# Optimization experiments

Hardware: AMD Instinct MI355X
Metric: run time of the kernel (lower is better)

## Reference

```python
import jax, jax.numpy as jnp
import numpy as np

TEMP = 0.2
NUM_PATCH, BATCH, DIM = 16, 512, 2048


def _l2_normalize(x, axis=-1, eps=1e-12):
    # matches torch F.normalize: x / max(||x||, eps)
    norm = jnp.linalg.norm(x, axis=axis, keepdims=True)
    return x / jnp.maximum(norm, eps)


def setup_inputs() -> dict:
    key = jax.random.key(0)
    features = jax.random.normal(key, (NUM_PATCH, BATCH, DIM), dtype=jnp.float32)
    return {"features": features}


def reference(features) -> jnp.ndarray:
    P, B, D = features.shape
    # z_avg: mean over the num_patch crops -> [B, D]
    z_avg = _l2_normalize(features.mean(axis=0), axis=1)
    # concat crops along batch -> [P*B, D], then L2 normalize rows
    f = _l2_normalize(features.reshape(P * B, D), axis=1)
    # similarity matrix [P*B, B]
    sim = f @ z_avg.T
    # labels = identity(B) tiled P times along rows => positive of row i is column i % B.
    # CE with target 0 after concat([pos, negs]) == -pos/T + logsumexp(all/T)
    rows = jnp.arange(P * B)
    pos = sim[rows, rows % B]
    logits = sim / TEMP
    loss = jnp.mean(jax.nn.logsumexp(logits, axis=1) - pos / TEMP)
    return loss
```

## Files before the change

kernel.cpp:

```cpp
#include <hip/hip_runtime.h>
#include <hip/hip_bf16.h>
#include <math.h>

#define NP 16
#define NB 512
#define ND 2048
#define NM (NP*NB)
#define BM 64
#define BN 128
#define BK 64
#define NS (ND/BK)
#define NCB (NB/BN)

typedef __attribute__((ext_vector_type(4))) float f32x4;
typedef unsigned int u32;

__device__ inline float dot4(float4 v) {
    return v.x * v.x + v.y * v.y + v.z * v.z + v.w * v.w;
}

#if __has_builtin(__builtin_amdgcn_cvt_pk_fp8_f32)
__device__ inline u32 pack4_fp8(float a, float b, float c, float d) {
    int w = 0;
    w = __builtin_amdgcn_cvt_pk_fp8_f32(a, b, w, false);
    w = __builtin_amdgcn_cvt_pk_fp8_f32(c, d, w, true);
    return (u32)w;
}
#else
#include <hip/hip_fp8.h>
__device__ inline u32 pack4_fp8(float a, float b, float c, float d) {
    u32 w  = (u32)__hip_cvt_float_to_fp8(a, __HIP_SATFINITE, __HIP_E4M3);
    w |= (u32)__hip_cvt_float_to_fp8(b, __HIP_SATFINITE, __HIP_E4M3) << 8;
    w |= (u32)__hip_cvt_float_to_fp8(c, __HIP_SATFINITE, __HIP_E4M3) << 16;
    w |= (u32)__hip_cvt_float_to_fp8(d, __HIP_SATFINITE, __HIP_E4M3) << 24;
    return w;
}
#endif

__global__ __launch_bounds__(512) void prep_kernel(
        const float* __restrict__ feat,
        unsigned char* __restrict__ an,
        unsigned char* __restrict__ zn) {
    const int b = blockIdx.x, tid = threadIdx.x;
    const int lane = tid & 63, wv = tid >> 6;
    const float4* feat4 = (const float4*)feat;

    float4 zp[8];
#pragma unroll
    for (int it = 0; it < 8; ++it) zp[it] = make_float4(0.f, 0.f, 0.f, 0.f);

#pragma unroll
    for (int j = 0; j < 2; ++j) {
        const int p = wv * 2 + j;
        const size_t row = (size_t)p * NB + b;
        const float4* rp = feat4 + row * (ND / 4);
        float4 rv[8];
        float ss = 0.f;
#pragma unroll
        for (int it = 0; it < 8; ++it) {
            rv[it] = rp[it * 64 + lane];
            ss += dot4(rv[it]);
            zp[it].x += rv[it].x; zp[it].y += rv[it].y;
            zp[it].z += rv[it].z; zp[it].w += rv[it].w;
        }
#pragma unroll
        for (int off = 32; off > 0; off >>= 1) ss += __shfl_xor(ss, off);
        const float inv = 1.f / fmaxf(sqrtf(ss), 1e-12f);
        u32* wp = (u32*)(an + row * ND);
#pragma unroll
        for (int it = 0; it < 8; ++it)
            wp[it * 64 + lane] = pack4_fp8(rv[it].x * inv, rv[it].y * inv,
                                           rv[it].z * inv, rv[it].w * inv);
    }

    __shared__ float4 zl[8][512];
#pragma unroll
    for (int it = 0; it < 8; ++it) zl[wv][it * 64 + lane] = zp[it];
    __syncthreads();

    float4 z = zl[0][tid];
#pragma unroll
    for (int v = 1; v < 8; ++v) {
        float4 t = zl[v][tid];
        z.x += t.x; z.y += t.y; z.z += t.z; z.w += t.w;
    }
    float ss = dot4(z);
#pragma unroll
    for (int off = 32; off > 0; off >>= 1) ss += __shfl_xor(ss, off);
    __shared__ float wpart[8];
    __shared__ float invz_s;
    if (lane == 0) wpart[wv] = ss;
    __syncthreads();
    if (tid == 0) {
        float t = 0.f;
#pragma unroll
        for (int v = 0; v < 8; ++v) t += wpart[v];
        invz_s = 1.f / fmaxf(sqrtf(t), 1e-12f);
    }
    __syncthreads();
    const float iz = invz_s;
    ((u32*)(zn + (size_t)b * ND))[tid] =
        pack4_fp8(z.x * iz, z.y * iz, z.z * iz, z.w * iz);
}

__global__ __launch_bounds__(256, 2) void gemm_loss_kernel(
        const unsigned char* __restrict__ an,
        const unsigned char* __restrict__ zn,
        float* __restrict__ pmax_g,
        float* __restrict__ psum_g,
        float* __restrict__ ppos_g) {
    __shared__ __align__(16) unsigned char abuf[3 * BM * BK];
    __shared__ __align__(16) unsigned char bbuf[3 * BN * BK];
    __shared__ float sm_max[BM][2];
    __shared__ float sm_sum[BM][2];
    __shared__ float sm_pos[BM];

    const int tid  = threadIdx.x;
    const int lane = tid & 63;
    const int w    = tid >> 6;
    const int wr   = w >> 1;
    const int wc   = w & 1;
    const int l15  = lane & 15;
    const int l4   = lane >> 4;
    const int cb   = blockIdx.x & (NCB - 1);
    const int brow = (blockIdx.x >> 2) * BM;
    const int bcol = cb * BN;

    f32x4 acc[2][4] = {};

    const int sra = tid >> 2;
    const int sca = (tid & 3) ^ ((sra >> 2) & 3);
    const unsigned char* asrc = an + (size_t)(brow + sra) * ND + sca * 16;
    const unsigned char* bsrc0;
    const unsigned char* bsrc1;
    {
        int q0 = tid, q1 = 256 + tid;
        int r0 = q0 >> 2, c0 = (q0 & 3) ^ ((r0 >> 2) & 3);
        int r1 = q1 >> 2, c1 = (q1 & 3) ^ ((r1 >> 2) & 3);
        bsrc0 = zn + (size_t)(bcol + r0) * ND + c0 * 16;
        bsrc1 = zn + (size_t)(bcol + r1) * ND + c1 * 16;
    }

#define STAGE(BI, S) do {                                                     \
        const int koB_ = (S) * BK;                                            \
        __builtin_amdgcn_global_load_lds((const u32*)(asrc + koB_),           \
            (u32*)(&abuf[(BI) * 4096 + tid * 16]), 16, 0, 0);                 \
        __builtin_amdgcn_global_load_lds((const u32*)(bsrc0 + koB_),          \
            (u32*)(&bbuf[(BI) * 8192 + tid * 16]), 16, 0, 0);                 \
        __builtin_amdgcn_global_load_lds((const u32*)(bsrc1 + koB_),          \
            (u32*)(&bbuf[(BI) * 8192 + 4096 + tid * 16]), 16, 0, 0);          \
    } while (0)

    STAGE(0, 0);
    STAGE(1, 1);

    int acur = 0, astg = 2;
    for (int s = 0; s < NS; ++s) {
        if (s + 1 < NS) asm volatile("s_waitcnt vmcnt(3)" ::: "memory");
        else            asm volatile("s_waitcnt vmcnt(0)" ::: "memory");
        __builtin_amdgcn_sched_barrier(0);
        __builtin_amdgcn_s_barrier();
        __builtin_amdgcn_sched_barrier(0);

        long long af[2][2], bf[2][4];
#pragma unroll
        for (int kc = 0; kc < 2; ++kc) {
            const int kk = kc * 4 + l4;
#pragma unroll
            for (int m = 0; m < 2; ++m) {
                int r = wr * 32 + m * 16 + l15;
                int g = (kk >> 1) ^ ((r >> 2) & 3);
                af[kc][m] = *(const long long*)(
                    &abuf[acur * 4096 + r * 64 + g * 16 + (kk & 1) * 8]);
            }
#pragma unroll
            for (int n = 0; n < 4; ++n) {
                int r = wc * 64 + n * 16 + l15;
                int g = (kk >> 1) ^ ((r >> 2) & 3);
                bf[kc][n] = *(const long long*)(
                    &bbuf[acur * 8192 + r * 64 + g * 16 + (kk & 1) * 8]);
            }
        }

        if (s + 2 < NS) STAGE(astg, s + 2);

        __builtin_amdgcn_s_setprio(1);
#pragma unroll
        for (int kc = 0; kc < 2; ++kc)
#pragma unroll
        for (int m = 0; m < 2; ++m)
#pragma unroll
        for (int n = 0; n < 4; ++n)
            acc[m][n] = __builtin_amdgcn_mfma_f32_16x16x32_fp8_fp8(
                af[kc][m], bf[kc][n], acc[m][n], 0, 0, 0);
        __builtin_amdgcn_s_setprio(0);

        acur = (acur == 2) ? 0 : acur + 1;
        astg = (astg == 2) ? 0 : astg + 1;
    }
#undef STAGE

#pragma unroll
    for (int m = 0; m < 2; ++m) {
#pragma unroll
        for (int r = 0; r < 4; ++r) {
            const int lrow = wr * 32 + m * 16 + l4 * 4 + r;
            float lg[4];
            float mx = -1e30f;
#pragma unroll
            for (int n = 0; n < 4; ++n) {
                lg[n] = acc[m][n][r] * 5.0f;
                mx = fmaxf(mx, lg[n]);
            }
            mx = fmaxf(mx, __shfl_xor(mx, 1));
            mx = fmaxf(mx, __shfl_xor(mx, 2));
            mx = fmaxf(mx, __shfl_xor(mx, 4));
            mx = fmaxf(mx, __shfl_xor(mx, 8));
            float se = 0.f;
#pragma unroll
            for (int n = 0; n < 4; ++n) se += __expf(lg[n] - mx);
            se += __shfl_xor(se, 1);
            se += __shfl_xor(se, 2);
            se += __shfl_xor(se, 4);
            se += __shfl_xor(se, 8);
            if (l15 == 0) { sm_max[lrow][wc] = mx; sm_sum[lrow][wc] = se; }
            const int posc = (brow + lrow) & (NB - 1);
#pragma unroll
            for (int n = 0; n < 4; ++n)
                if (bcol + wc * 64 + n * 16 + l15 == posc) sm_pos[lrow] = lg[n];
        }
    }
    __syncthreads();

    if (tid < BM) {
        const int lrow = tid;
        const int grow = brow + lrow;
        const float m0 = sm_max[lrow][0], m1 = sm_max[lrow][1];
        const float gm = fmaxf(m0, m1);
        const float tot = sm_sum[lrow][0] * __expf(m0 - gm)
                        + sm_sum[lrow][1] * __expf(m1 - gm);
        pmax_g[cb * NM + grow] = gm;
        psum_g[cb * NM + grow] = tot;
        if (((grow & (NB - 1)) >> 7) == cb) ppos_g[grow] = sm_pos[lrow];
    }
}

__global__ __launch_bounds__(256) void reduce_kernel(
        const float* __restrict__ pmax_g, const float* __restrict__ psum_g,
        const float* __restrict__ ppos_g, float* __restrict__ acc_g,
        u32* __restrict__ counter, float* __restrict__ out) {
    const int row = blockIdx.x * 256 + threadIdx.x;
    float mxs[NCB];
    float gm = -1e30f;
#pragma unroll
    for (int c = 0; c < NCB; ++c) {
        mxs[c] = pmax_g[c * NM + row];
        gm = fmaxf(gm, mxs[c]);
    }
    float tot = 0.f;
#pragma unroll
    for (int c = 0; c < NCB; ++c)
        tot += psum_g[c * NM + row] * __expf(mxs[c] - gm);
    float term = gm + __logf(tot) - ppos_g[row];
#pragma unroll
    for (int off = 32; off > 0; off >>= 1) term += __shfl_xor(term, off);
    __shared__ float wsum[4];
    const int lane = threadIdx.x & 63, wv = threadIdx.x >> 6;
    if (lane == 0) wsum[wv] = term;
    __syncthreads();
    if (threadIdx.x == 0) {
        atomicAdd(acc_g, wsum[0] + wsum[1] + wsum[2] + wsum[3]);
        __threadfence();
        u32 old = atomicAdd(counter, 1u);
        if (old == 31u) {
            float total = atomicAdd(acc_g, 0.0f);
            out[0] = total * (1.0f / (float)NM);
        }
    }
}

extern "C" void kernel_launch(void* const* d_in, const int* in_sizes, int n_in,
                              void* d_out, int out_size, void* d_ws, size_t ws_size,
                              hipStream_t stream) {
    const float* feat = (const float*)d_in[0];

    unsigned char* an = (unsigned char*)d_ws;
    unsigned char* zn = an + (size_t)NM * ND;
    float* pmax = (float*)(zn + (size_t)NB * ND);
    float* psum = pmax + NCB * NM;
    float* ppos = psum + NCB * NM;
    float* accg = ppos + NM;
    u32*   cntr = (u32*)(accg + 1);

    hipMemsetAsync(accg, 0, 8, stream);

    prep_kernel<<<NB, 512, 0, stream>>>(feat, an, zn);
    gemm_loss_kernel<<<(NM / BM) * NCB, 256, 0, stream>>>(an, zn, pmax, psum, ppos);
    reduce_kernel<<<NM / 256, 256, 0, stream>>>(pmax, psum, ppos, accg, cntr,
                                                (float*)d_out);
}
```

Before: 48.14 us.

## Restructure prep kernel to per-column patch loop and fold memset into kernel

The prep kernel is reorganised so that each thread owns one float4 column slice and loads all 16 patches for it. The patch mean then accumulates in registers with no shared-memory cross-wave reduction. Per-row sums of squares are reduced through a small shared array, so the 32KB shared buffer goes away. The separate hipMemsetAsync that zeroed the accumulator and counter is replaced by a write inside the prep kernel, removing one launch. The trade-off is more register pressure from holding 16 float4s and more scattered global stores per row.

```diff
diff --git a/kernel.cpp b/kernel.cpp
--- a/kernel.cpp
+++ b/kernel.cpp
@@ -40,66 +40,61 @@
 __global__ __launch_bounds__(512) void prep_kernel(
         const float* __restrict__ feat,
         unsigned char* __restrict__ an,
-        unsigned char* __restrict__ zn) {
+        unsigned char* __restrict__ zn,
+        float* __restrict__ accg, u32* __restrict__ cntr) {
     const int b = blockIdx.x, tid = threadIdx.x;
     const int lane = tid & 63, wv = tid >> 6;
-    const float4* feat4 = (const float4*)feat;
-
-    float4 zp[8];
-#pragma unroll
-    for (int it = 0; it < 8; ++it) zp[it] = make_float4(0.f, 0.f, 0.f, 0.f);
-
-#pragma unroll
-    for (int j = 0; j < 2; ++j) {
-        const int p = wv * 2 + j;
-        const size_t row = (size_t)p * NB + b;
-        const float4* rp = feat4 + row * (ND / 4);
-        float4 rv[8];
-        float ss = 0.f;
-#pragma unroll
-        for (int it = 0; it < 8; ++it) {
-            rv[it] = rp[it * 64 + lane];
-            ss += dot4(rv[it]);
-            zp[it].x += rv[it].x; zp[it].y += rv[it].y;
-            zp[it].z += rv[it].z; zp[it].w += rv[it].w;
-        }
+    if (b == 0 && tid == 0) { accg[0] = 0.f; cntr[0] = 0u; }
+
+    const int dbase = wv * 256 + lane * 4;
+    const float4* fp4 = (const float4*)feat;
+
+    float4 rv[16];
+    float4 z = make_float4(0.f, 0.f, 0.f, 0.f);
+#pragma unroll
+    for (int p = 0; p < NP; ++p) {
+        rv[p] = fp4[((size_t)(p * NB + b) * ND + dbase) >> 2];
+        z.x += rv[p].x; z.y += rv[p].y; z.z += rv[p].z; z.w += rv[p].w;
+    }
+
+    __shared__ float sm_ssq[NP][8];
+    __shared__ float sm_z[8];
+    __shared__ float sm_inv[NP + 1];
+#pragma unroll
+    for (int p = 0; p < NP; ++p) {
+        float ss = dot4(rv[p]);
 #pragma unroll
         for (int off = 32; off > 0; off >>= 1) ss += __shfl_xor(ss, off);
-        const float inv = 1.f / fmaxf(sqrtf(ss), 1e-12f);
-        u32* wp = (u32*)(an + row * ND);
-#pragma unroll
-        for (int it = 0; it < 8; ++it)
-            wp[it * 64 + lane] = pack4_fp8(rv[it].x * inv, rv[it].y * inv,
-                                           rv[it].z * inv, rv[it].w * inv);
-    }
-
-    __shared__ float4 zl[8][512];
-#pragma unroll
-    for (int it = 0; it < 8; ++it) zl[wv][it * 64 + lane] = zp[it];
-    __syncthreads();
-
-    float4 z = zl[0][tid];
-#pragma unroll
-    for (int v = 1; v < 8; ++v) {
-        float4 t = zl[v][tid];
-        z.x += t.x; z.y += t.y; z.z += t.z; z.w += t.w;
-    }
-    float ss = dot4(z);
-#pragma unroll
-    for (int off = 32; off > 0; off >>= 1) ss += __shfl_xor(ss, off);
-    __shared__ float wpart[8];
-    __shared__ float invz_s;
-    if (lane == 0) wpart[wv] = ss;
-    __syncthreads();
-    if (tid == 0) {
+        if (lane == 0) sm_ssq[p][wv] = ss;
+    }
+    {
+        float zs = dot4(z);
+#pragma unroll
+        for (int off = 32; off > 0; off >>= 1) zs += __shfl_xor(zs, off);
+        if (lane == 0) sm_z[wv] = zs;
+    }
+    __syncthreads();
+    if (tid < NP) {
         float t = 0.f;
 #pragma unroll
-        for (int v = 0; v < 8; ++v) t += wpart[v];
-        invz_s = 1.f / fmaxf(sqrtf(t), 1e-12f);
-    }
-    __syncthreads();
-    const float iz = invz_s;
-    ((u32*)(zn + (size_t)b * ND))[tid] =
+        for (int v = 0; v < 8; ++v) t += sm_ssq[tid][v];
+        sm_inv[tid] = 1.f / fmaxf(sqrtf(t), 1e-12f);
+    } else if (tid == NP) {
+        float t = 0.f;
+#pragma unroll
+        for (int v = 0; v < 8; ++v) t += sm_z[v];
+        sm_inv[NP] = 1.f / fmaxf(sqrtf(t), 1e-12f);
+    }
+    __syncthreads();
+
+#pragma unroll
+    for (int p = 0; p < NP; ++p) {
+        const float inv = sm_inv[p];
+        ((u32*)(an + (size_t)(p * NB + b) * ND))[dbase >> 2] =
+            pack4_fp8(rv[p].x * inv, rv[p].y * inv, rv[p].z * inv, rv[p].w * inv);
+    }
+    const float iz = sm_inv[NP];
+    ((u32*)(zn + (size_t)b * ND))[dbase >> 2] =
         pack4_fp8(z.x * iz, z.y * iz, z.z * iz, z.w * iz);
 }
 
@@ -292,9 +287,7 @@
     float* accg = ppos + NM;
     u32*   cntr = (u32*)(accg + 1);
 
-    hipMemsetAsync(accg, 0, 8, stream);
-
-    prep_kernel<<<NB, 512, 0, stream>>>(feat, an, zn);
+    prep_kernel<<<NB, 512, 0, stream>>>(feat, an, zn, accg, cntr);
     gemm_loss_kernel<<<(NM / BM) * NCB, 256, 0, stream>>>(an, zn, pmax, psum, ppos);
     reduce_kernel<<<NM / 256, 256, 0, stream>>>(pmax, psum, ppos, accg, cntr,
                                                 (float*)d_out);
```

Result: faster. 46.54 us (-3.3%).
